# Kernel tuning notes

Hardware: AMD Instinct MI355X
Metric: run time of the kernel (lower is better)

The kernel has to match this reference:

```python
import jax, jax.numpy as jnp
import numpy as np

B, T, L_IN, D, H = 8, 8192, 1536, 768, 8
E = D // H  # 96 = per-head feature dim


def _resize_linear(x, out_size):
    """F.interpolate(mode='linear', align_corners=True) along last dim."""
    L = x.shape[-1]
    pos = jnp.arange(out_size, dtype=jnp.float32) * ((L - 1) / (out_size - 1))
    i0 = jnp.floor(pos).astype(jnp.int32)
    i1 = jnp.minimum(i0 + 1, L - 1)
    w = (pos - i0.astype(jnp.float32)).astype(x.dtype)
    return x[..., i0] * (1.0 - w) + x[..., i1] * w


def setup_inputs() -> dict:
    key = jax.random.key(0)
    ks = jax.random.split(key, 8)
    s_e = 1.0 / np.sqrt(E)
    return {
        "x": jax.random.normal(ks[0], (B, T, L_IN), dtype=jnp.float32),
        "lens": jnp.full((B,), L_IN, dtype=jnp.int32),
        "ln_gamma": jnp.ones((D,), dtype=jnp.float32),
        "ln_beta": jnp.zeros((D,), dtype=jnp.float32),
        "Wa": jax.random.normal(ks[1], (H, E, E), dtype=jnp.float32) * s_e,
        "ba": jax.random.normal(ks[2], (H, E), dtype=jnp.float32) * s_e,
        "Wb": jax.random.normal(ks[3], (H, E, E), dtype=jnp.float32) * s_e,
        "bb": jax.random.normal(ks[4], (H, E), dtype=jnp.float32) * s_e,
        "Wc": jax.random.normal(ks[5], (H, E), dtype=jnp.float32) * s_e,
        "bc": jax.random.normal(ks[6], (H,), dtype=jnp.float32) * s_e,
    }


def reference(x, lens, ln_gamma, ln_beta, Wa, ba, Wb, bb, Wc, bc):
    # Per-sample ragged resize to 768 features (lens uniform == x.shape[-1]).
    xr = _resize_linear(x, D)                                # [B, T, 768]
    # LayerNorm(embed_dim)
    mu = xr.mean(-1, keepdims=True)
    var = xr.var(-1, keepdims=True)
    xn = (xr - mu) * jax.lax.rsqrt(var + 1e-5) * ln_gamma + ln_beta
    # rearrange 'b t (e c) -> b t e c' with c = num_heads
    h = xn.reshape(B, T, E, H)
    # Gated ABMIL per head (dropout = identity at eval), vectorized over heads
    a = jnp.tanh(jnp.einsum('bteh,hef->btfh', h, Wa) + ba.T)          # [B,T,E,H]
    g = jax.nn.sigmoid(jnp.einsum('bteh,hef->btfh', h, Wb) + bb.T)    # [B,T,E,H]
    A_raw = jnp.einsum('btfh,hf->bth', a * g, Wc) + bc                # [B,T,H]
    # stack heads, mean over heads, softmax over tokens
    A = jax.nn.softmax(A_raw.mean(-1), axis=-1)                       # [B,T]
    # per-sample attention pooling: feat_i = A_i @ x_i
    feats = jnp.einsum('bt,btf->bf', A, xn)                           # [B,768]
    return feats
```

## Files before the change

### kernel.cpp

```cpp
#include <hip/hip_runtime.h>
#include <math.h>

#define B_    8
#define T_    8192
#define LIN   1536
#define D_    768
#define H_    8
#define E_    96
#define TT    16
#define NWA   8192
#define BPB   (T_ / TT)

typedef float f32x4 __attribute__((ext_vector_type(4)));
typedef short s16x8 __attribute__((ext_vector_type(8)));
typedef short s16x4 __attribute__((ext_vector_type(4)));

static __device__ __forceinline__ short f2bf(float f) {
    unsigned u = __float_as_uint(f);
    unsigned r = (u + 0x7FFFu + ((u >> 16) & 1u)) >> 16;
    return (short)r;
}
static __device__ __forceinline__ float bf2f(short s) {
    return __uint_as_float(((unsigned)(unsigned short)s) << 16);
}
static __device__ __forceinline__ float fused_gate(float a, float g) {
    float ta = __expf(-2.0f * a);
    float tg = __expf(-g);
    return (1.0f - ta) * __builtin_amdgcn_rcpf((1.0f + ta) * (1.0f + tg));
}

__global__ __launch_bounds__(256)
void k0_wprep(const float* __restrict__ Wa, const float* __restrict__ Wb,
              short* __restrict__ wtA, short* __restrict__ wtB)
{
    int o = blockIdx.x * 256 + threadIdx.x;
    if (o >= H_ * E_ * E_) return;
    int e = o % E_;
    int f = (o / E_) % E_;
    int h = o / (E_ * E_);
    int in = h * E_ * E_ + e * E_ + f;
    wtA[o] = f2bf(Wa[in]);
    wtB[o] = f2bf(Wb[in]);
}

__global__ __launch_bounds__(256)
void kA_resln(const float* __restrict__ x,
              const float* __restrict__ gamma, const float* __restrict__ beta,
              short* __restrict__ xnb)
{
    const int tid  = threadIdx.x;
    const int lane = tid & 63;
    const int wv   = tid >> 6;
    const int gw   = blockIdx.x * 4 + wv;

    const float SCALE = (float)(1535.0 / 767.0);
    float gm[12], btv[12], wl[12];
    #pragma unroll
    for (int c = 0; c < 3; ++c)
        #pragma unroll
        for (int d = 0; d < 4; ++d) {
            int k = 4 * c + d;
            int j = 256 * c + 4 * lane + d;
            float pos = (float)j * SCALE;
            int a = (int)floorf(pos);
            if (a > LIN - 1) a = LIN - 1;
            wl[k] = pos - (float)a;
            gm[k]  = gamma[j];
            btv[k] = beta[j];
        }
    const bool last = (lane == 63);

    const size_t tok0 = (size_t)gw * 8;
    const float* base = x + tok0 * LIN;

    f32x4 La0 = *(const f32x4*)&base[           8 * lane];
    f32x4 Lb0 = *(const f32x4*)&base[           8 * lane + 4];
    f32x4 La1 = *(const f32x4*)&base[512  +     8 * lane];
    f32x4 Lb1 = *(const f32x4*)&base[512  +     8 * lane + 4];
    f32x4 La2 = *(const f32x4*)&base[1024 +     8 * lane];
    f32x4 Lb2 = *(const f32x4*)&base[1024 +     8 * lane + 4];

    #pragma unroll
    for (int tt = 0; tt < 8; ++tt) {
        f32x4 Na0, Nb0, Na1, Nb1, Na2, Nb2;
        if (tt < 7) {
            const float* nr = base + (size_t)(tt + 1) * LIN;
            Na0 = *(const f32x4*)&nr[           8 * lane];
            Nb0 = *(const f32x4*)&nr[           8 * lane + 4];
            Na1 = *(const f32x4*)&nr[512  +     8 * lane];
            Nb1 = *(const f32x4*)&nr[512  +     8 * lane + 4];
            Na2 = *(const f32x4*)&nr[1024 +     8 * lane];
            Nb2 = *(const f32x4*)&nr[1024 +     8 * lane + 4];
        }

        float xr[12];
        float sum = 0.0f, ssq = 0.0f;
        #pragma unroll
        for (int c = 0; c < 3; ++c) {
            f32x4 A = (c == 0) ? La0 : (c == 1) ? La1 : La2;
            f32x4 Bv = (c == 0) ? Lb0 : (c == 1) ? Lb1 : Lb2;
            #pragma unroll
            for (int d = 0; d < 4; ++d) {
                int k = 4 * c + d;
                int idx = (d & 1) * 2;
                float lo = (d < 2) ? A[idx]     : Bv[idx];
                float hi = (d < 2) ? A[idx + 1] : Bv[idx + 1];
                if (c == 2 && d == 3 && last && wl[k] == 0.0f)
                    lo = Lb2[3];
                float v = lo * (1.0f - wl[k]) + hi * wl[k];
                xr[k] = v; sum += v; ssq = fmaf(v, v, ssq);
            }
        }

        #pragma unroll
        for (int o = 1; o < 64; o <<= 1) {
            sum += __shfl_xor(sum, o, 64);
            ssq += __shfl_xor(ssq, o, 64);
        }
        float mu = sum * (1.0f / D_);
        float rs = 1.0f / sqrtf(ssq * (1.0f / D_) - mu * mu + 1e-5f);

        short* dst = xnb + (tok0 + tt) * D_;
        #pragma unroll
        for (int c = 0; c < 3; ++c) {
            s16x4 p;
            #pragma unroll
            for (int d = 0; d < 4; ++d) {
                int k = 4 * c + d;
                p[d] = f2bf((xr[k] - mu) * rs * gm[k] + btv[k]);
            }
            *(s16x4*)&dst[256 * c + 4 * lane] = p;
        }

        if (tt < 7) {
            La0 = Na0; Lb0 = Nb0; La1 = Na1; Lb1 = Nb1; La2 = Na2; Lb2 = Nb2;
        }
    }
}

__global__ __launch_bounds__(256)
void kB_score(const short* __restrict__ xnb,
              const short* __restrict__ wtA, const short* __restrict__ wtB,
              const float* __restrict__ ba, const float* __restrict__ bb,
              const float* __restrict__ Wc, const float* __restrict__ bc,
              float* __restrict__ partial, float* __restrict__ mzb)
{
    __shared__ __align__(16) short xnt[TT * D_];
    __shared__ float red2[TT][4];
    __shared__ float scs[TT];
    __shared__ float wsh[TT];

    const int bid  = blockIdx.x;
    const int tid  = threadIdx.x;
    const int lane = tid & 63;
    const int wv   = tid >> 6;
    const int bt0  = bid * TT;

    #pragma unroll
    for (int i = 0; i < 6; ++i) {
        int chunk = i * 256 + tid;
        int tok   = chunk / 96;
        int e     = chunk % 96;
        s16x8 v = *(const s16x8*)&xnb[(size_t)(bt0 + tok) * D_ + e * 8];
        int base = tok * D_;
        int swz  = (tok & 7) << 3;
        #pragma unroll
        for (int h = 0; h < 8; ++h) {
            int sidx = (base + h * E_ + e) ^ swz;
            xnt[sidx] = v[h];
        }
    }
    __syncthreads();

    const int ln15 = lane & 15;
    const int q    = lane >> 4;
    const int tokA = ln15;
    const int swzA = (tokA & 7) << 3;

    float hacc[4] = {0.0f, 0.0f, 0.0f, 0.0f};

    #pragma unroll
    for (int hh = 0; hh < 2; ++hh) {
        const int h = wv * 2 + hh;
        s16x8 afr[3];
        #pragma unroll
        for (int kk = 0; kk < 3; ++kk) {
            int sidx = (tokA * D_ + h * E_ + kk * 32 + q * 8) ^ swzA;
            afr[kk] = *(const s16x8*)&xnt[sidx];
        }
        f32x4 accA[6], accG[6];
        #pragma unroll
        for (int nt = 0; nt < 6; ++nt) {
            accA[nt] = (f32x4){0.f, 0.f, 0.f, 0.f};
            accG[nt] = (f32x4){0.f, 0.f, 0.f, 0.f};
        }
        #pragma unroll
        for (int nt = 0; nt < 6; ++nt) {
            const short* rowA = wtA + h * (E_ * E_) + (nt * 16 + ln15) * E_ + q * 8;
            const short* rowB = wtB + h * (E_ * E_) + (nt * 16 + ln15) * E_ + q * 8;
            #pragma unroll
            for (int kk = 0; kk < 3; ++kk) {
                s16x8 bA = *(const s16x8*)(rowA + kk * 32);
                s16x8 bG = *(const s16x8*)(rowB + kk * 32);
                accA[nt] = __builtin_amdgcn_mfma_f32_16x16x32_bf16(afr[kk], bA, accA[nt], 0, 0, 0);
                accG[nt] = __builtin_amdgcn_mfma_f32_16x16x32_bf16(afr[kk], bG, accG[nt], 0, 0, 0);
            }
        }
        float v0 = 0.f, v1 = 0.f, v2 = 0.f, v3 = 0.f;
        #pragma unroll
        for (int nt = 0; nt < 6; ++nt) {
            int f = nt * 16 + ln15;
            float bav = ba[h * E_ + f];
            float bbv = bb[h * E_ + f];
            float wcv = Wc[h * E_ + f];
            v0 += fused_gate(accA[nt][0] + bav, accG[nt][0] + bbv) * wcv;
            v1 += fused_gate(accA[nt][1] + bav, accG[nt][1] + bbv) * wcv;
            v2 += fused_gate(accA[nt][2] + bav, accG[nt][2] + bbv) * wcv;
            v3 += fused_gate(accA[nt][3] + bav, accG[nt][3] + bbv) * wcv;
        }
        hacc[0] += v0; hacc[1] += v1; hacc[2] += v2; hacc[3] += v3;
    }

    #pragma unroll
    for (int r = 0; r < 4; ++r) {
        float v = hacc[r];
        v += __shfl_xor(v, 1, 64);
        v += __shfl_xor(v, 2, 64);
        v += __shfl_xor(v, 4, 64);
        v += __shfl_xor(v, 8, 64);
        hacc[r] = v;
    }
    if (ln15 == 0) {
        #pragma unroll
        for (int r = 0; r < 4; ++r)
            red2[q * 4 + r][wv] = hacc[r];
    }
    __syncthreads();

    if (tid < TT) {
        float bcsum = 0.0f;
        #pragma unroll
        for (int h2 = 0; h2 < H_; ++h2) bcsum += bc[h2];
        scs[tid] = (red2[tid][0] + red2[tid][1] + red2[tid][2] + red2[tid][3]
                    + bcsum) * (1.0f / H_);
    }
    __syncthreads();

    float mb = scs[0];
    #pragma unroll
    for (int t = 1; t < TT; ++t) mb = fmaxf(mb, scs[t]);
    if (tid < TT) wsh[tid] = __expf(scs[tid] - mb);
    __syncthreads();

    if (tid == 0) {
        float zb = 0.0f;
        #pragma unroll
        for (int t = 0; t < TT; ++t) zb += wsh[t];
        mzb[bid * 2]     = mb;
        mzb[bid * 2 + 1] = zb;
    }

    float wt[TT];
    #pragma unroll
    for (int t = 0; t < TT; ++t) wt[t] = wsh[t];

    float* pp = partial + (size_t)bid * D_;
    #pragma unroll
    for (int kk = 0; kk < 3; ++kk) {
        int jp = kk * 256 + tid;
        float a = 0.0f;
        #pragma unroll
        for (int t = 0; t < TT; ++t)
            a = fmaf(wt[t], bf2f(xnt[(t * D_ + jp) ^ ((t & 7) << 3)]), a);
        pp[jp] = a;
    }
}

__global__ __launch_bounds__(256)
void kMZ(const float* __restrict__ mzb, float* __restrict__ MZ)
{
    __shared__ float red[8];
    __shared__ float Msh;
    const int b = blockIdx.x, tid = threadIdx.x, lane = tid & 63, wv = tid >> 6;
    const float* p = mzb + (size_t)b * BPB * 2;

    float m0 = p[tid * 2], m1 = p[(tid + 256) * 2];
    float z0 = p[tid * 2 + 1], z1 = p[(tid + 256) * 2 + 1];

    float M = fmaxf(m0, m1);
    #pragma unroll
    for (int o = 32; o > 0; o >>= 1) M = fmaxf(M, __shfl_down(M, o, 64));
    if (lane == 0) red[wv] = M;
    __syncthreads();
    if (tid == 0) Msh = fmaxf(fmaxf(red[0], red[1]), fmaxf(red[2], red[3]));
    __syncthreads();
    M = Msh;

    float Z = z0 * __expf(m0 - M) + z1 * __expf(m1 - M);
    #pragma unroll
    for (int o = 32; o > 0; o >>= 1) Z += __shfl_down(Z, o, 64);
    if (lane == 0) red[wv] = Z;
    __syncthreads();
    if (tid == 0) {
        float z = red[0] + red[1] + red[2] + red[3];
        MZ[b * 2]     = M;
        MZ[b * 2 + 1] = 1.0f / z;
    }
}

__global__ __launch_bounds__(256)
void k4_reduce(const float* __restrict__ partial, const float* __restrict__ mzb,
               const float* __restrict__ MZ, float* __restrict__ out)
{
    __shared__ float sc[BPB];
    const int b = blockIdx.x / 3, third = blockIdx.x % 3, tid = threadIdx.x;
    const float M = MZ[b * 2], Zinv = MZ[b * 2 + 1];

    const float* pm = mzb + (size_t)b * BPB * 2;
    sc[tid]       = __expf(pm[tid * 2] - M) * Zinv;
    sc[tid + 256] = __expf(pm[(tid + 256) * 2] - M) * Zinv;
    __syncthreads();

    const int jp = third * 256 + tid;
    const float* pp = partial + (size_t)b * BPB * D_ + jp;
    float sum = 0.0f;
    for (int c = 0; c < BPB; ++c)
        sum = fmaf(pp[(size_t)c * D_], sc[c], sum);

    int h = jp / 96, e = jp % 96;
    out[b * D_ + e * 8 + h] = sum;
}

extern "C" void kernel_launch(void* const* d_in, const int* in_sizes, int n_in,
                              void* d_out, int out_size, void* d_ws, size_t ws_size,
                              hipStream_t stream)
{
    const float* x     = (const float*)d_in[0];
    const float* gamma = (const float*)d_in[2];
    const float* beta  = (const float*)d_in[3];
    const float* Wa    = (const float*)d_in[4];
    const float* ba    = (const float*)d_in[5];
    const float* Wb    = (const float*)d_in[6];
    const float* bb    = (const float*)d_in[7];
    const float* Wc    = (const float*)d_in[8];
    const float* bc    = (const float*)d_in[9];
    float* out = (float*)d_out;

    float* ws      = (float*)d_ws;
    float* partial = ws;
    float* mzb     = partial + (size_t)B_ * BPB * D_;
    float* MZ      = mzb + (size_t)B_ * BPB * 2;
    short* wtA     = (short*)(MZ + 16);
    short* wtB     = wtA + H_ * E_ * E_;
    short* xnb     = wtB + H_ * E_ * E_;

    hipLaunchKernelGGL(k0_wprep, dim3((H_ * E_ * E_ + 255) / 256), dim3(256), 0, stream,
                       Wa, Wb, wtA, wtB);
    hipLaunchKernelGGL(kA_resln, dim3(NWA / 4), dim3(256), 0, stream,
                       x, gamma, beta, xnb);
    hipLaunchKernelGGL(kB_score, dim3(B_ * T_ / TT), dim3(256), 0, stream,
                       xnb, wtA, wtB, ba, bb, Wc, bc, partial, mzb);
    hipLaunchKernelGGL(kMZ, dim3(B_), dim3(256), 0, stream, mzb, MZ);
    hipLaunchKernelGGL(k4_reduce, dim3(B_ * 3), dim3(256), 0, stream,
                       partial, mzb, MZ, out);
}
```

Baseline: 215.2 us.

## Fuse resize+LayerNorm into score kernel, writing normalized tokens straight to LDS

Merges the resize/LayerNorm kernel into the gated-attention scoring kernel. Each wave now normalizes 4 of the block's 16 tokens and writes the bf16 results directly into the swizzled shared-memory tile instead of round-tripping a bf16 xnb buffer through global memory. This removes one kernel launch and the global write and re-read of the normalized activations (about 100 MB of traffic). In exchange the fused kernel carries more registers and its LDS writes become scalar 2-byte stores with a scattered layout, which may cause bank conflicts and lower occupancy.

```diff
diff --git a/kernel.cpp b/kernel.cpp
--- a/kernel.cpp
+++ b/kernel.cpp
@@ -8,7 +8,6 @@
 #define H_    8
 #define E_    96
 #define TT    16
-#define NWA   8192
 #define BPB   (T_ / TT)
 
 typedef float f32x4 __attribute__((ext_vector_type(4)));
@@ -44,102 +43,8 @@
 }
 
 __global__ __launch_bounds__(256)
-void kA_resln(const float* __restrict__ x,
+void kF_fused(const float* __restrict__ x,
               const float* __restrict__ gamma, const float* __restrict__ beta,
-              short* __restrict__ xnb)
-{
-    const int tid  = threadIdx.x;
-    const int lane = tid & 63;
-    const int wv   = tid >> 6;
-    const int gw   = blockIdx.x * 4 + wv;
-
-    const float SCALE = (float)(1535.0 / 767.0);
-    float gm[12], btv[12], wl[12];
-    #pragma unroll
-    for (int c = 0; c < 3; ++c)
-        #pragma unroll
-        for (int d = 0; d < 4; ++d) {
-            int k = 4 * c + d;
-            int j = 256 * c + 4 * lane + d;
-            float pos = (float)j * SCALE;
-            int a = (int)floorf(pos);
-            if (a > LIN - 1) a = LIN - 1;
-            wl[k] = pos - (float)a;
-            gm[k]  = gamma[j];
-            btv[k] = beta[j];
-        }
-    const bool last = (lane == 63);
-
-    const size_t tok0 = (size_t)gw * 8;
-    const float* base = x + tok0 * LIN;
-
-    f32x4 La0 = *(const f32x4*)&base[           8 * lane];
-    f32x4 Lb0 = *(const f32x4*)&base[           8 * lane + 4];
-    f32x4 La1 = *(const f32x4*)&base[512  +     8 * lane];
-    f32x4 Lb1 = *(const f32x4*)&base[512  +     8 * lane + 4];
-    f32x4 La2 = *(const f32x4*)&base[1024 +     8 * lane];
-    f32x4 Lb2 = *(const f32x4*)&base[1024 +     8 * lane + 4];
-
-    #pragma unroll
-    for (int tt = 0; tt < 8; ++tt) {
-        f32x4 Na0, Nb0, Na1, Nb1, Na2, Nb2;
-        if (tt < 7) {
-            const float* nr = base + (size_t)(tt + 1) * LIN;
-            Na0 = *(const f32x4*)&nr[           8 * lane];
-            Nb0 = *(const f32x4*)&nr[           8 * lane + 4];
-            Na1 = *(const f32x4*)&nr[512  +     8 * lane];
-            Nb1 = *(const f32x4*)&nr[512  +     8 * lane + 4];
-            Na2 = *(const f32x4*)&nr[1024 +     8 * lane];
-            Nb2 = *(const f32x4*)&nr[1024 +     8 * lane + 4];
-        }
-
-        float xr[12];
-        float sum = 0.0f, ssq = 0.0f;
-        #pragma unroll
-        for (int c = 0; c < 3; ++c) {
-            f32x4 A = (c == 0) ? La0 : (c == 1) ? La1 : La2;
-            f32x4 Bv = (c == 0) ? Lb0 : (c == 1) ? Lb1 : Lb2;
-            #pragma unroll
-            for (int d = 0; d < 4; ++d) {
-                int k = 4 * c + d;
-                int idx = (d & 1) * 2;
-                float lo = (d < 2) ? A[idx]     : Bv[idx];
-                float hi = (d < 2) ? A[idx + 1] : Bv[idx + 1];
-                if (c == 2 && d == 3 && last && wl[k] == 0.0f)
-                    lo = Lb2[3];
-                float v = lo * (1.0f - wl[k]) + hi * wl[k];
-                xr[k] = v; sum += v; ssq = fmaf(v, v, ssq);
-            }
-        }
-
-        #pragma unroll
-        for (int o = 1; o < 64; o <<= 1) {
-            sum += __shfl_xor(sum, o, 64);
-            ssq += __shfl_xor(ssq, o, 64);
-        }
-        float mu = sum * (1.0f / D_);
-        float rs = 1.0f / sqrtf(ssq * (1.0f / D_) - mu * mu + 1e-5f);
-
-        short* dst = xnb + (tok0 + tt) * D_;
-        #pragma unroll
-        for (int c = 0; c < 3; ++c) {
-            s16x4 p;
-            #pragma unroll
-            for (int d = 0; d < 4; ++d) {
-                int k = 4 * c + d;
-                p[d] = f2bf((xr[k] - mu) * rs * gm[k] + btv[k]);
-            }
-            *(s16x4*)&dst[256 * c + 4 * lane] = p;
-        }
-
-        if (tt < 7) {
-            La0 = Na0; Lb0 = Nb0; La1 = Na1; Lb1 = Nb1; La2 = Na2; Lb2 = Nb2;
-        }
-    }
-}
-
-__global__ __launch_bounds__(256)
-void kB_score(const short* __restrict__ xnb,
               const short* __restrict__ wtA, const short* __restrict__ wtB,
               const float* __restrict__ ba, const float* __restrict__ bb,
               const float* __restrict__ Wc, const float* __restrict__ bc,
@@ -156,18 +61,87 @@
     const int wv   = tid >> 6;
     const int bt0  = bid * TT;
 
-    #pragma unroll
-    for (int i = 0; i < 6; ++i) {
-        int chunk = i * 256 + tid;
-        int tok   = chunk / 96;
-        int e     = chunk % 96;
-        s16x8 v = *(const s16x8*)&xnb[(size_t)(bt0 + tok) * D_ + e * 8];
-        int base = tok * D_;
-        int swz  = (tok & 7) << 3;
-        #pragma unroll
-        for (int h = 0; h < 8; ++h) {
-            int sidx = (base + h * E_ + e) ^ swz;
-            xnt[sidx] = v[h];
+    {
+        const float SCALE = (float)(1535.0 / 767.0);
+        float gm[12], btv[12], wl[12];
+        int   dst0[12];
+        #pragma unroll
+        for (int c = 0; c < 3; ++c)
+            #pragma unroll
+            for (int d = 0; d < 4; ++d) {
+                int k = 4 * c + d;
+                int j = 256 * c + 4 * lane + d;
+                float pos = (float)j * SCALE;
+                int a = (int)floorf(pos);
+                if (a > LIN - 1) a = LIN - 1;
+                wl[k] = pos - (float)a;
+                gm[k]  = gamma[j];
+                btv[k] = beta[j];
+                dst0[k] = (j & 7) * E_ + (j >> 3);
+            }
+        const bool last = (lane == 63);
+
+        const int t0 = wv * 4;
+        const float* base = x + (size_t)(bt0 + t0) * LIN;
+
+        f32x4 La0 = *(const f32x4*)&base[           8 * lane];
+        f32x4 Lb0 = *(const f32x4*)&base[           8 * lane + 4];
+        f32x4 La1 = *(const f32x4*)&base[512  +     8 * lane];
+        f32x4 Lb1 = *(const f32x4*)&base[512  +     8 * lane + 4];
+        f32x4 La2 = *(const f32x4*)&base[1024 +     8 * lane];
+        f32x4 Lb2 = *(const f32x4*)&base[1024 +     8 * lane + 4];
+
+        #pragma unroll
+        for (int tt = 0; tt < 4; ++tt) {
+            f32x4 Na0, Nb0, Na1, Nb1, Na2, Nb2;
+            if (tt < 3) {
+                const float* nr = base + (size_t)(tt + 1) * LIN;
+                Na0 = *(const f32x4*)&nr[           8 * lane];
+                Nb0 = *(const f32x4*)&nr[           8 * lane + 4];
+                Na1 = *(const f32x4*)&nr[512  +     8 * lane];
+                Nb1 = *(const f32x4*)&nr[512  +     8 * lane + 4];
+                Na2 = *(const f32x4*)&nr[1024 +     8 * lane];
+                Nb2 = *(const f32x4*)&nr[1024 +     8 * lane + 4];
+            }
+
+            float xr[12];
+            float sum = 0.0f, ssq = 0.0f;
+            #pragma unroll
+            for (int c = 0; c < 3; ++c) {
+                f32x4 A  = (c == 0) ? La0 : (c == 1) ? La1 : La2;
+                f32x4 Bv = (c == 0) ? Lb0 : (c == 1) ? Lb1 : Lb2;
+                #pragma unroll
+                for (int d = 0; d < 4; ++d) {
+                    int k = 4 * c + d;
+                    int idx = (d & 1) * 2;
+                    float lo = (d < 2) ? A[idx]     : Bv[idx];
+                    float hi = (d < 2) ? A[idx + 1] : Bv[idx + 1];
+                    if (c == 2 && d == 3 && last && wl[k] == 0.0f)
+                        lo = Lb2[3];
+                    float v = lo * (1.0f - wl[k]) + hi * wl[k];
+                    xr[k] = v; sum += v; ssq = fmaf(v, v, ssq);
+                }
+            }
+
+            #pragma unroll
+            for (int o = 1; o < 64; o <<= 1) {
+                sum += __shfl_xor(sum, o, 64);
+                ssq += __shfl_xor(ssq, o, 64);
+            }
+            float mu = sum * (1.0f / D_);
+            float rs = 1.0f / sqrtf(ssq * (1.0f / D_) - mu * mu + 1e-5f);
+
+            const int tok = t0 + tt;
+            const int swz = (tok & 7) << 3;
+            #pragma unroll
+            for (int k = 0; k < 12; ++k) {
+                int sidx = (tok * D_ + dst0[k]) ^ swz;
+                xnt[sidx] = f2bf((xr[k] - mu) * rs * gm[k] + btv[k]);
+            }
+
+            if (tt < 3) {
+                La0 = Na0; Lb0 = Nb0; La1 = Na1; Lb1 = Nb1; La2 = Na2; Lb2 = Nb2;
+            }
         }
     }
     __syncthreads();
@@ -352,14 +326,11 @@
     float* MZ      = mzb + (size_t)B_ * BPB * 2;
     short* wtA     = (short*)(MZ + 16);
     short* wtB     = wtA + H_ * E_ * E_;
-    short* xnb     = wtB + H_ * E_ * E_;
 
     hipLaunchKernelGGL(k0_wprep, dim3((H_ * E_ * E_ + 255) / 256), dim3(256), 0, stream,
                        Wa, Wb, wtA, wtB);
-    hipLaunchKernelGGL(kA_resln, dim3(NWA / 4), dim3(256), 0, stream,
-                       x, gamma, beta, xnb);
-    hipLaunchKernelGGL(kB_score, dim3(B_ * T_ / TT), dim3(256), 0, stream,
-                       xnb, wtA, wtB, ba, bb, Wc, bc, partial, mzb);
+    hipLaunchKernelGGL(kF_fused, dim3(B_ * T_ / TT), dim3(256), 0, stream,
+                       x, gamma, beta, wtA, wtB, ba, bb, Wc, bc, partial, mzb);
     hipLaunchKernelGGL(kMZ, dim3(B_), dim3(256), 0, stream, mzb, MZ);
     hipLaunchKernelGGL(k4_reduce, dim3(B_ * 3), dim3(256), 0, stream,
                        partial, mzb, MZ, out);
```

Measured after the change: 175.2 us. 18.6% less time.
